# Kernel tuning notes

Hardware: AMD Instinct MI355X
Metric: run time of the kernel (lower is better)

The kernel has to match this reference:

```python
import jax, jax.numpy as jnp
import numpy as np

N = 50000   # num nodes
E = 400000  # num edges (avg degree 8)
D = 256     # in_channels
H = 256     # hidden_channels
C = 64      # out_channels
K = 2       # k_hops


def setup_inputs() -> dict:
    key = jax.random.key(0)
    ks = jax.random.split(key, 10)
    x = jax.random.normal(ks[0], (N, D), dtype=jnp.float32)
    edge_index = jax.random.randint(ks[1], (2, E), 0, N, dtype=jnp.int32)
    s = 0.05
    # per-hop linears of the single H2GCNConv (weights stored [in, out])
    W0 = jax.random.normal(ks[2], (D, H), jnp.float32) * s
    W1 = jax.random.normal(ks[3], (D, H), jnp.float32) * s
    W2 = jax.random.normal(ks[4], (D, H), jnp.float32) * s
    b0 = jnp.zeros((H,), jnp.float32)
    b1 = jnp.zeros((H,), jnp.float32)
    b2 = jnp.zeros((H,), jnp.float32)
    # classifier: h2_out_dim = H*(K+1) = 768 -> C
    Wc = jax.random.normal(ks[5], (H * (K + 1), C), jnp.float32) * s
    bc = jnp.zeros((C,), jnp.float32)
    return {"x": x, "edge_index": edge_index, "num_nodes": N,
            "W0": W0, "b0": b0, "W1": W1, "b1": b1, "W2": W2, "b2": b2,
            "Wc": Wc, "bc": bc}


def _normalize_adj(edge_index, num_nodes):
    # add self loops, then D^{-1/2} A D^{-1/2} edge weights
    loops = jnp.arange(num_nodes, dtype=edge_index.dtype)
    ei = jnp.concatenate([edge_index, jnp.stack([loops, loops])], axis=1)
    row, col = ei[0], ei[1]
    deg = jax.ops.segment_sum(jnp.ones(row.shape[0], jnp.float32), row,
                              num_segments=num_nodes)
    dis = jnp.where(deg > 0, deg ** -0.5, 0.0)  # inf -> 0 for isolated nodes
    return ei, dis[row] * dis[col]


def _sparse_mm(edge_index, edge_weight, x, num_nodes):
    # gather -> scale -> scatter-add (COO SpMM)
    row, col = edge_index[0], edge_index[1]
    msg = x[col] * edge_weight[:, None]  # [E', F]
    return jax.ops.segment_sum(msg, row, num_segments=num_nodes)


def reference(x, edge_index, num_nodes, W0, b0, W1, b1, W2, b2, Wc, bc):
    ei, ew = _normalize_adj(edge_index, num_nodes)
    # H2GCNConv: ego + k-hop aggregates, each through its own linear, concat
    outs = [x @ W0 + b0]
    cur = x
    for Wk, bk in ((W1, b1), (W2, b2)):
        cur = _sparse_mm(ei, ew, cur, num_nodes)
        outs.append(cur @ Wk + bk)
    h = jax.nn.relu(jnp.concatenate(outs, axis=1))  # [N, 3H]
    # dropout p=0 / eval mode -> identity
    return h @ Wc + bc
```

## Files before the change

### kernel.cpp

```cpp
#include <hip/hip_runtime.h>


#define FD 256
#define CO 64
#define SB 512
#define MT1 391
#define PS (50048 * 256)

using frag_ab = __attribute__((ext_vector_type(8))) short;
using f32x4   = __attribute__((ext_vector_type(4))) float;
typedef unsigned short u16;
typedef unsigned int   u32;

__device__ __forceinline__ u16 f2bf(float f) {
    u32 u = __builtin_bit_cast(u32, f);
    return (u16)((u + 0x7FFFu + ((u >> 16) & 1u)) >> 16);
}
__device__ __forceinline__ float bfl(u32 packed) {
    return __builtin_bit_cast(float, packed << 16);
}
__device__ __forceinline__ float bfh(u32 packed) {
    return __builtin_bit_cast(float, packed & 0xFFFF0000u);
}

__device__ __forceinline__ void gll16(const void* g, void* l) {
    __builtin_amdgcn_global_load_lds(
        (const __attribute__((address_space(1))) u32*)g,
        (__attribute__((address_space(3))) u32*)l, 16, 0, 0);
}

#define BAR()  __builtin_amdgcn_s_barrier()
#define WLG0() asm volatile("s_waitcnt lgkmcnt(0)" ::: "memory")
#define WVM0() asm volatile("s_waitcnt vmcnt(0)" ::: "memory")
#define WVM2() asm volatile("s_waitcnt vmcnt(2)" ::: "memory")

__global__ void init_kernel(int* deg, int* fill, int n) {
    int i = blockIdx.x * blockDim.x + threadIdx.x;
    if (i < n) { deg[i] = 1; fill[i] = 0; }
}
__global__ void count_kernel(const int* __restrict__ ei0, int* deg, int e) {
    int i = blockIdx.x * blockDim.x + threadIdx.x;
    if (i < e) atomicAdd(&deg[ei0[i]], 1);
}
__global__ void scan1(const int* __restrict__ deg, int* __restrict__ rowptr,
                      int* __restrict__ bsum, float* __restrict__ dis, int n) {
    __shared__ int sh[SB];
    int tid = threadIdx.x;
    int i = blockIdx.x * SB + tid;
    int v = (i < n) ? deg[i] : 0;
    if (i < n) dis[i] = rsqrtf((float)v);
    sh[tid] = v;
    __syncthreads();
    for (int off = 1; off < SB; off <<= 1) {
        int add = (tid >= off) ? sh[tid - off] : 0;
        __syncthreads();
        sh[tid] += add;
        __syncthreads();
    }
    if (i < n) rowptr[i] = sh[tid] - v;
    if (tid == SB - 1) bsum[blockIdx.x] = sh[tid];
}
__global__ void scan2(const int* __restrict__ bsum, int* __restrict__ bscan, int nb) {
    __shared__ int sh[128];
    int tid = threadIdx.x;
    int v = (tid < nb) ? bsum[tid] : 0;
    sh[tid] = v;
    __syncthreads();
    for (int off = 1; off < 128; off <<= 1) {
        int add = (tid >= off) ? sh[tid - off] : 0;
        __syncthreads();
        sh[tid] += add;
        __syncthreads();
    }
    if (tid < nb) bscan[tid] = sh[tid] - v;
    if (tid == nb - 1) bscan[nb] = sh[tid];
}
__global__ void scan3(int* rowptr, const int* __restrict__ bscan, int n, int nb) {
    int i = blockIdx.x * 256 + threadIdx.x;
    if (i < n) rowptr[i] += bscan[i / SB];
    if (i == n) rowptr[n] = bscan[nb];
}
__global__ void fill_kernel(const int* __restrict__ ei, const float* __restrict__ dis,
                            const int* __restrict__ rowptr, int* fill,
                            int2* __restrict__ cw, int e, int n) {
    int i = blockIdx.x * blockDim.x + threadIdx.x;
    if (i >= e + n) return;
    int r, c;
    if (i < e) { r = ei[i]; c = ei[e + i]; }
    else       { r = i - e; c = r; }
    float w = dis[r] * dis[c];
    int pos = rowptr[r] + atomicAdd(&fill[r], 1);
    int2 p; p.x = c; p.y = __float_as_int(w);
    cw[pos] = p;
}

__global__ void conv_kernel(const float* __restrict__ x, u16* __restrict__ xb, int total4) {
    int i = blockIdx.x * blockDim.x + threadIdx.x;
    if (i < total4) {
        float4 v = ((const float4*)x)[i];
        ushort4 o;
        o.x = f2bf(v.x); o.y = f2bf(v.y); o.z = f2bf(v.z); o.w = f2bf(v.w);
        ((ushort4*)xb)[i] = o;
    }
}
__global__ void wtrans_kernel(const float* __restrict__ W0, const float* __restrict__ W1,
                              const float* __restrict__ W2, const float* __restrict__ Wc,
                              u16* __restrict__ WkT, u16* __restrict__ WcT) {
    __shared__ u16 tl[64][65];
    int b = blockIdx.x;
    const float* src; u16* dst; int R, C, r0, c0;
    if (b < 48) {
        int k = b >> 4, t = b & 15;
        src = (k == 0) ? W0 : (k == 1) ? W1 : W2;
        dst = WkT + k * 65536;
        R = 256; C = 256; r0 = (t >> 2) * 64; c0 = (t & 3) * 64;
    } else {
        int t = b - 48;
        src = Wc; dst = WcT;
        R = 768; C = 64; r0 = t * 64; c0 = 0;
    }
    int tid = threadIdx.x;
    int rr = tid >> 4, cc = (tid & 15) * 4;
    #pragma unroll
    for (int it = 0; it < 4; ++it) {
        int r = it * 16 + rr;
        float4 v = *(const float4*)(src + (size_t)(r0 + r) * C + c0 + cc);
        tl[cc + 0][r] = f2bf(v.x); tl[cc + 1][r] = f2bf(v.y);
        tl[cc + 2][r] = f2bf(v.z); tl[cc + 3][r] = f2bf(v.w);
    }
    __syncthreads();
    #pragma unroll
    for (int it = 0; it < 4; ++it) {
        int crow = it * 16 + rr;
        ushort4 o;
        o.x = tl[crow][cc + 0]; o.y = tl[crow][cc + 1];
        o.z = tl[crow][cc + 2]; o.w = tl[crow][cc + 3];
        *(ushort4*)(dst + (size_t)(c0 + crow) * R + r0 + cc) = o;
    }
}

__global__ void spmm_bf16(const int* __restrict__ rowptr, const int2* __restrict__ cw,
                          const u16* __restrict__ xb, u16* __restrict__ outb, int n) {
    int tid = threadIdx.x;
    int lane = tid & 63;
    int row = blockIdx.x * 8 + ((tid >> 6) << 1) + (lane >> 5);
    if (row >= n) return;
    int l32 = lane & 31;
    int p0 = rowptr[row], p1 = rowptr[row + 1];
    float a[8];
    #pragma unroll
    for (int j = 0; j < 8; ++j) a[j] = 0.f;

    int p = p0;
    for (; p + 8 <= p1; p += 8) {
        int2 cwv[8]; uint4 v[8];
        #pragma unroll
        for (int u = 0; u < 8; ++u) cwv[u] = cw[p + u];
        #pragma unroll
        for (int u = 0; u < 8; ++u)
            v[u] = *(const uint4*)(xb + (size_t)cwv[u].x * FD + l32 * 8);
        #pragma unroll
        for (int u = 0; u < 8; ++u) {
            float wt = __int_as_float(cwv[u].y);
            a[0] += wt * bfl(v[u].x); a[1] += wt * bfh(v[u].x);
            a[2] += wt * bfl(v[u].y); a[3] += wt * bfh(v[u].y);
            a[4] += wt * bfl(v[u].z); a[5] += wt * bfh(v[u].z);
            a[6] += wt * bfl(v[u].w); a[7] += wt * bfh(v[u].w);
        }
    }
    for (; p + 2 <= p1; p += 2) {
        int2 cwv[2]; uint4 v[2];
        #pragma unroll
        for (int u = 0; u < 2; ++u) cwv[u] = cw[p + u];
        #pragma unroll
        for (int u = 0; u < 2; ++u)
            v[u] = *(const uint4*)(xb + (size_t)cwv[u].x * FD + l32 * 8);
        #pragma unroll
        for (int u = 0; u < 2; ++u) {
            float wt = __int_as_float(cwv[u].y);
            a[0] += wt * bfl(v[u].x); a[1] += wt * bfh(v[u].x);
            a[2] += wt * bfl(v[u].y); a[3] += wt * bfh(v[u].y);
            a[4] += wt * bfl(v[u].z); a[5] += wt * bfh(v[u].z);
            a[6] += wt * bfl(v[u].w); a[7] += wt * bfh(v[u].w);
        }
    }
    for (; p < p1; ++p) {
        int2 cwv = cw[p];
        float wt = __int_as_float(cwv.y);
        uint4 v = *(const uint4*)(xb + (size_t)cwv.x * FD + l32 * 8);
        a[0] += wt * bfl(v.x); a[1] += wt * bfh(v.x);
        a[2] += wt * bfl(v.y); a[3] += wt * bfh(v.y);
        a[4] += wt * bfl(v.z); a[5] += wt * bfh(v.z);
        a[6] += wt * bfl(v.w); a[7] += wt * bfh(v.w);
    }
    uint4 o;
    o.x = (u32)f2bf(a[0]) | ((u32)f2bf(a[1]) << 16);
    o.y = (u32)f2bf(a[2]) | ((u32)f2bf(a[3]) << 16);
    o.z = (u32)f2bf(a[4]) | ((u32)f2bf(a[5]) << 16);
    o.w = (u32)f2bf(a[6]) | ((u32)f2bf(a[7]) << 16);
    *(uint4*)(outb + (size_t)row * FD + l32 * 8) = o;
}

__launch_bounds__(256, 3)
__global__ void gemm1(const u16* __restrict__ xb, const u16* __restrict__ agg1b,
                      const u16* __restrict__ agg2b, const u16* __restrict__ WkT,
                      const float* __restrict__ b0, const float* __restrict__ b1,
                      const float* __restrict__ b2, u16* __restrict__ T, int n) {
    __shared__ __align__(16) char lds[32768];
    char* lA = lds;
    char* lB = lds + 16384;

    const int tid = threadIdx.x;
    const int w = tid >> 6, l = tid & 63;
    const int l4 = l >> 4, lm = l & 15;
    const int mq = w & 1, nq = w >> 1;

    int bid = blockIdx.x;
    const int nt  = bid & 1;
    int rest = bid >> 1;
    const int mt  = rest % MT1;
    const int seg = rest / MT1;
    const int row0 = mt * 128;
    const int n0   = nt * 128;

    const u16* inb = (seg == 0) ? xb : (seg == 1) ? agg1b : agg2b;
    const u16* WT  = WkT + (size_t)seg * 65536;
    const float* bk = (seg == 0) ? b0 : (seg == 1) ? b1 : b2;

    f32x4 acc[4][4];
    #pragma unroll
    for (int jm = 0; jm < 4; ++jm)
        #pragma unroll
        for (int rn = 0; rn < 4; ++rn) acc[jm][rn] = (f32x4)(0.f);

    for (int kt = 0; kt < 4; ++kt) {
        WLG0();
        BAR();
        #pragma unroll
        for (int c = 0; c < 4; ++c) {
            int L = w * 1024 + c * 4096 + l * 16;
            int r = L >> 7, s = (L >> 4) & 7;
            int k16 = s ^ (r & 7);
            int gr = row0 + r; if (gr > n - 1) gr = n - 1;
            gll16(inb + (size_t)gr * FD + kt * 64 + k16 * 8, lA + w * 1024 + c * 4096);
        }
        #pragma unroll
        for (int c = 0; c < 4; ++c) {
            int L = w * 1024 + c * 4096 + l * 16;
            int r = L >> 7, s = (L >> 4) & 7;
            int k16 = s ^ (r & 7);
            gll16(WT + (size_t)(n0 + r) * FD + kt * 64 + k16 * 8, lB + w * 1024 + c * 4096);
        }
        WVM0();
        BAR();

        #pragma unroll
        for (int kk2 = 0; kk2 < 2; ++kk2) {
            frag_ab af[4], bf_[4];
            #pragma unroll
            for (int jm = 0; jm < 4; ++jm) {
                int rB = nq * 64 + jm * 16 + lm;
                af[jm] = *(const frag_ab*)(lB + rB * 128 + (((kk2 * 4 + l4) ^ (rB & 7)) << 4));
            }
            #pragma unroll
            for (int rn = 0; rn < 4; ++rn) {
                int rA = mq * 64 + rn * 16 + lm;
                bf_[rn] = *(const frag_ab*)(lA + rA * 128 + (((kk2 * 4 + l4) ^ (rA & 7)) << 4));
            }
            #pragma unroll
            for (int jm = 0; jm < 4; ++jm)
                #pragma unroll
                for (int rn = 0; rn < 4; ++rn)
                    acc[jm][rn] = __builtin_amdgcn_mfma_f32_16x16x32_bf16(af[jm], bf_[rn], acc[jm][rn], 0, 0, 0);
        }
    }
    WLG0();
    BAR();

    #pragma unroll
    for (int jm = 0; jm < 4; ++jm) {
        int j = nq * 64 + jm * 16 + l4 * 4;
        float4 bb = *(const float4*)(bk + n0 + j);
        #pragma unroll
        for (int rn = 0; rn < 4; ++rn) {
            int r = mq * 64 + rn * 16 + lm;
            f32x4 v = acc[jm][rn];
            ushort4 p;
            p.x = f2bf(fmaxf(v[0] + bb.x, 0.f));
            p.y = f2bf(fmaxf(v[1] + bb.y, 0.f));
            p.z = f2bf(fmaxf(v[2] + bb.z, 0.f));
            p.w = f2bf(fmaxf(v[3] + bb.w, 0.f));
            *(ushort4*)(lds + r * 256 + (((j >> 3) ^ (r & 7)) << 4) + (j & 7) * 2) = p;
        }
    }
    WLG0();
    BAR();

    u16* Tp = T + (size_t)seg * PS;
    {
        const int c16 = tid & 15;
        #pragma unroll
        for (int i = 0; i < 8; ++i) {
            int r = i * 16 + (tid >> 4);
            uint4 v = *(const uint4*)(lds + r * 256 + ((c16 ^ (r & 7)) << 4));
            *(uint4*)(Tp + (size_t)(row0 + r) * FD + n0 + c16 * 8) = v;
        }
    }
}

__launch_bounds__(256, 3)
__global__ void gemm2(const u16* __restrict__ T, const u16* __restrict__ WcT,
                      const float* __restrict__ bc, float* __restrict__ out, int n) {
    __shared__ __align__(16) char lds[16384];
    const int tid = threadIdx.x;
    const int w = tid >> 6, l = tid & 63;
    const int l4 = l >> 4, lm = l & 15;
    const int row0 = blockIdx.x * 64;
    const int rr = w * 16 + lm;
    const int r  = row0 + rr;

    frag_ab b[24];
    #pragma unroll
    for (int kt = 0; kt < 12; ++kt)
        #pragma unroll
        for (int kk2 = 0; kk2 < 2; ++kk2)
            b[kt * 2 + kk2] = *(const frag_ab*)(T + (size_t)(kt >> 2) * PS +
                                                (size_t)r * FD + (kt & 3) * 64 + kk2 * 32 + l4 * 8);

    auto stageW = [&](int kt, char* buf) {
        #pragma unroll
        for (int i = 0; i < 2; ++i) {
            int L = tid * 16 + i * 4096;
            int c = L >> 7, s = (L >> 4) & 7;
            gll16(WcT + (size_t)c * 768 + kt * 64 + (s ^ (c & 7)) * 8,
                  buf + w * 1024 + i * 4096);
        }
    };

    f32x4 acc[4];
    #pragma unroll
    for (int am = 0; am < 4; ++am) acc[am] = (f32x4)(0.f);

    stageW(0, lds);
    #pragma unroll
    for (int kt = 0; kt < 12; ++kt) {
        char* cur = lds + (kt & 1) * 8192;
        if (kt < 11) {
            stageW(kt + 1, lds + ((kt + 1) & 1) * 8192);
            WVM2();
        } else {
            WVM0();
        }
        BAR();
        #pragma unroll
        for (int kk2 = 0; kk2 < 2; ++kk2) {
            #pragma unroll
            for (int am = 0; am < 4; ++am) {
                int c = am * 16 + lm;
                frag_ab afr = *(const frag_ab*)(cur + c * 128 + (((kk2 * 4 + l4) ^ (c & 7)) << 4));
                acc[am] = __builtin_amdgcn_mfma_f32_16x16x32_bf16(afr, b[kt * 2 + kk2], acc[am], 0, 0, 0);
            }
        }
        WLG0();
        BAR();
    }

    if (r < n) {
        #pragma unroll
        for (int am = 0; am < 4; ++am) {
            float4 bb = *(const float4*)(bc + am * 16 + l4 * 4);
            float4 o;
            o.x = acc[am][0] + bb.x;
            o.y = acc[am][1] + bb.y;
            o.z = acc[am][2] + bb.z;
            o.w = acc[am][3] + bb.w;
            *(float4*)(out + (size_t)r * CO + am * 16 + l4 * 4) = o;
        }
    }
}

extern "C" void kernel_launch(void* const* d_in, const int* in_sizes, int n_in,
                              void* d_out, int out_size, void* d_ws, size_t ws_size,
                              hipStream_t stream) {
    const float* x  = (const float*)d_in[0];
    const int*   ei = (const int*)d_in[1];
    const float* W0 = (const float*)d_in[3];
    const float* b0 = (const float*)d_in[4];
    const float* W1 = (const float*)d_in[5];
    const float* b1 = (const float*)d_in[6];
    const float* W2 = (const float*)d_in[7];
    const float* b2 = (const float*)d_in[8];
    const float* Wc = (const float*)d_in[9];
    const float* bc = (const float*)d_in[10];
    float* out = (float*)d_out;

    const int n  = in_sizes[0] / FD;
    const int e  = in_sizes[1] / 2;
    const int ep = e + n;
    const int nb = (n + SB - 1) / SB;

    char* ws = (char*)d_ws;
    size_t o = 0;
    auto take = [&](size_t nbytes) -> char* {
        char* p = ws + o;
        o += (nbytes + 255) & ~(size_t)255;
        return p;
    };
    int*   deg    = (int*)  take((size_t)n * 4);
    int*   fill   = (int*)  take((size_t)n * 4);
    float* dis    = (float*)take((size_t)n * 4);
    int*   rowptr = (int*)  take((size_t)(n + 1) * 4);
    int*   bsum   = (int*)  take((size_t)(nb + 1) * 4);
    int*   bscan  = (int*)  take((size_t)(nb + 1) * 4);
    int2*  cw     = (int2*) take((size_t)ep * 8);
    u16*   xb     = (u16*)  take((size_t)n * FD * 2);
    u16*   agg1b  = (u16*)  take((size_t)n * FD * 2);
    u16*   agg2b  = (u16*)  take((size_t)n * FD * 2);
    u16*   WkT    = (u16*)  take((size_t)3 * FD * FD * 2);
    u16*   WcT    = (u16*)  take((size_t)CO * 3 * FD * 2);
    u16*   T      = (u16*)  take((size_t)3 * PS * 2);
    (void)ws_size; (void)n_in; (void)out_size;

    init_kernel <<<(n + 255) / 256, 256, 0, stream>>>(deg, fill, n);
    count_kernel<<<(e + 255) / 256, 256, 0, stream>>>(ei, deg, e);
    scan1       <<<nb, SB, 0, stream>>>(deg, rowptr, bsum, dis, n);
    scan2       <<<1, 128, 0, stream>>>(bsum, bscan, nb);
    scan3       <<<(n + 256) / 256, 256, 0, stream>>>(rowptr, bscan, n, nb);
    fill_kernel <<<(ep + 255) / 256, 256, 0, stream>>>(ei, dis, rowptr, fill, cw, e, n);

    const int total4 = n * FD / 4;
    conv_kernel  <<<(total4 + 255) / 256, 256, 0, stream>>>(x, xb, total4);
    wtrans_kernel<<<60, 256, 0, stream>>>(W0, W1, W2, Wc, WkT, WcT);

    spmm_bf16<<<(n + 7) / 8, 256, 0, stream>>>(rowptr, cw, xb, agg1b, n);
    spmm_bf16<<<(n + 7) / 8, 256, 0, stream>>>(rowptr, cw, agg1b, agg2b, n);

    gemm1<<<2 * MT1 * 3, 256, 0, stream>>>(xb, agg1b, agg2b, WkT, b0, b1, b2, T, n);
    gemm2<<<(n + 63) / 64, 256, 0, stream>>>(T, WcT, bc, out, n);
}
```

Measured before the change: 211.0 us.

## Double-buffer gemm1 K-loop, remap blocks per XCD, replace init kernel with memsets

gemm1 now uses a double-buffered LDS pipeline: it splits K into eight 32-wide steps and prefetches the next tile with global_load_lds while the current tile feeds the MFMAs. The swizzle shrinks to 4 slots per 64-byte row. Block IDs are remapped so consecutive tiles land on the same XCD, which should improve L2 reuse of the weight tiles. Launch bounds rise to 4 waves per SIMD, and the init kernel becomes two hipMemsetAsync calls, with the self-loop +1 moved into scan1. The higher occupancy target may cause register spills.

```diff
diff --git a/kernel.cpp b/kernel.cpp
--- a/kernel.cpp
+++ b/kernel.cpp
@@ -34,10 +34,6 @@
 #define WVM0() asm volatile("s_waitcnt vmcnt(0)" ::: "memory")
 #define WVM2() asm volatile("s_waitcnt vmcnt(2)" ::: "memory")
 
-__global__ void init_kernel(int* deg, int* fill, int n) {
-    int i = blockIdx.x * blockDim.x + threadIdx.x;
-    if (i < n) { deg[i] = 1; fill[i] = 0; }
-}
 __global__ void count_kernel(const int* __restrict__ ei0, int* deg, int e) {
     int i = blockIdx.x * blockDim.x + threadIdx.x;
     if (i < e) atomicAdd(&deg[ei0[i]], 1);
@@ -47,7 +43,7 @@
     __shared__ int sh[SB];
     int tid = threadIdx.x;
     int i = blockIdx.x * SB + tid;
-    int v = (i < n) ? deg[i] : 0;
+    int v = (i < n) ? deg[i] + 1 : 0;
     if (i < n) dis[i] = rsqrtf((float)v);
     sh[tid] = v;
     __syncthreads();
@@ -201,21 +197,23 @@
     *(uint4*)(outb + (size_t)row * FD + l32 * 8) = o;
 }
 
-__launch_bounds__(256, 3)
+__launch_bounds__(256, 4)
 __global__ void gemm1(const u16* __restrict__ xb, const u16* __restrict__ agg1b,
                       const u16* __restrict__ agg2b, const u16* __restrict__ WkT,
                       const float* __restrict__ b0, const float* __restrict__ b1,
                       const float* __restrict__ b2, u16* __restrict__ T, int n) {
     __shared__ __align__(16) char lds[32768];
-    char* lA = lds;
-    char* lB = lds + 16384;
 
     const int tid = threadIdx.x;
     const int w = tid >> 6, l = tid & 63;
     const int l4 = l >> 4, lm = l & 15;
     const int mq = w & 1, nq = w >> 1;
 
-    int bid = blockIdx.x;
+    int nwg = gridDim.x;
+    int q8 = nwg >> 3, r8 = nwg & 7;
+    int xcd = blockIdx.x & 7, idx = blockIdx.x >> 3;
+    int bid = (xcd < r8 ? xcd * (q8 + 1) : r8 * (q8 + 1) + (xcd - r8) * q8) + idx;
+
     const int nt  = bid & 1;
     int rest = bid >> 1;
     const int mt  = rest % MT1;
@@ -227,55 +225,61 @@
     const u16* WT  = WkT + (size_t)seg * 65536;
     const float* bk = (seg == 0) ? b0 : (seg == 1) ? b1 : b2;
 
+    auto stage = [&](int kt, char* buf) {
+        #pragma unroll
+        for (int i = 0; i < 2; ++i) {
+            int L = w * 1024 + i * 4096 + l * 16;
+            int r = L >> 6, s = (L >> 4) & 3;
+            int k16 = s ^ (r & 3);
+            int gr = row0 + r; if (gr > n - 1) gr = n - 1;
+            gll16(inb + (size_t)gr * FD + kt * 32 + k16 * 8, buf + w * 1024 + i * 4096);
+        }
+        #pragma unroll
+        for (int i = 0; i < 2; ++i) {
+            int L = w * 1024 + i * 4096 + l * 16;
+            int r = L >> 6, s = (L >> 4) & 3;
+            int k16 = s ^ (r & 3);
+            gll16(WT + (size_t)(n0 + r) * FD + kt * 32 + k16 * 8,
+                  buf + 8192 + w * 1024 + i * 4096);
+        }
+    };
+
     f32x4 acc[4][4];
     #pragma unroll
     for (int jm = 0; jm < 4; ++jm)
         #pragma unroll
         for (int rn = 0; rn < 4; ++rn) acc[jm][rn] = (f32x4)(0.f);
 
-    for (int kt = 0; kt < 4; ++kt) {
+    stage(0, lds);
+    WVM0();
+    BAR();
+
+    #pragma unroll
+    for (int kt = 0; kt < 8; ++kt) {
+        char* cur = lds + (kt & 1) * 16384;
+        if (kt < 7) stage(kt + 1, lds + ((kt + 1) & 1) * 16384);
+
+        frag_ab af[4], bf_[4];
+        #pragma unroll
+        for (int jm = 0; jm < 4; ++jm) {
+            int rB = nq * 64 + jm * 16 + lm;
+            af[jm] = *(const frag_ab*)(cur + 8192 + rB * 64 + ((l4 ^ (rB & 3)) << 4));
+        }
+        #pragma unroll
+        for (int rn = 0; rn < 4; ++rn) {
+            int rA = mq * 64 + rn * 16 + lm;
+            bf_[rn] = *(const frag_ab*)(cur + rA * 64 + ((l4 ^ (rA & 3)) << 4));
+        }
+        #pragma unroll
+        for (int jm = 0; jm < 4; ++jm)
+            #pragma unroll
+            for (int rn = 0; rn < 4; ++rn)
+                acc[jm][rn] = __builtin_amdgcn_mfma_f32_16x16x32_bf16(af[jm], bf_[rn], acc[jm][rn], 0, 0, 0);
+
+        if (kt < 7) WVM0();
         WLG0();
         BAR();
-        #pragma unroll
-        for (int c = 0; c < 4; ++c) {
-            int L = w * 1024 + c * 4096 + l * 16;
-            int r = L >> 7, s = (L >> 4) & 7;
-            int k16 = s ^ (r & 7);
-            int gr = row0 + r; if (gr > n - 1) gr = n - 1;
-            gll16(inb + (size_t)gr * FD + kt * 64 + k16 * 8, lA + w * 1024 + c * 4096);
-        }
-        #pragma unroll
-        for (int c = 0; c < 4; ++c) {
-            int L = w * 1024 + c * 4096 + l * 16;
-            int r = L >> 7, s = (L >> 4) & 7;
-            int k16 = s ^ (r & 7);
-            gll16(WT + (size_t)(n0 + r) * FD + kt * 64 + k16 * 8, lB + w * 1024 + c * 4096);
-        }
-        WVM0();
-        BAR();
-
-        #pragma unroll
-        for (int kk2 = 0; kk2 < 2; ++kk2) {
-            frag_ab af[4], bf_[4];
-            #pragma unroll
-            for (int jm = 0; jm < 4; ++jm) {
-                int rB = nq * 64 + jm * 16 + lm;
-                af[jm] = *(const frag_ab*)(lB + rB * 128 + (((kk2 * 4 + l4) ^ (rB & 7)) << 4));
-            }
-            #pragma unroll
-            for (int rn = 0; rn < 4; ++rn) {
-                int rA = mq * 64 + rn * 16 + lm;
-                bf_[rn] = *(const frag_ab*)(lA + rA * 128 + (((kk2 * 4 + l4) ^ (rA & 7)) << 4));
-            }
-            #pragma unroll
-            for (int jm = 0; jm < 4; ++jm)
-                #pragma unroll
-                for (int rn = 0; rn < 4; ++rn)
-                    acc[jm][rn] = __builtin_amdgcn_mfma_f32_16x16x32_bf16(af[jm], bf_[rn], acc[jm][rn], 0, 0, 0);
-        }
-    }
-    WLG0();
-    BAR();
+    }
 
     #pragma unroll
     for (int jm = 0; jm < 4; ++jm) {
@@ -421,7 +425,8 @@
     u16*   T      = (u16*)  take((size_t)3 * PS * 2);
     (void)ws_size; (void)n_in; (void)out_size;
 
-    init_kernel <<<(n + 255) / 256, 256, 0, stream>>>(deg, fill, n);
+    hipMemsetAsync(deg,  0, (size_t)n * 4, stream);
+    hipMemsetAsync(fill, 0, (size_t)n * 4, stream);
     count_kernel<<<(e + 255) / 256, 256, 0, stream>>>(ei, deg, e);
     scan1       <<<nb, SB, 0, stream>>>(deg, rowptr, bsum, dis, n);
     scan2       <<<1, 128, 0, stream>>>(bsum, bscan, nb);
```

Result: faster. 205.8 us (-2.5%).
